# Kernel optimization log

Hardware: AMD Instinct MI355X
Metric: run time of the kernel (lower is better)

The kernel has to match this reference:

```python
import jax, jax.numpy as jnp
import numpy as np

B, S, d, D = 128, 1024, 64, 64  # batch, seq_len, physical dim, bond dim


def setup_inputs() -> dict:
    key = jax.random.key(0)
    k1, k2, k3, k4 = jax.random.split(key, 4)
    k_core = (d * D * D) ** (-0.5)
    k_vec = d ** (-0.5)
    core = k_core * jax.random.normal(k1, (d, D, D), dtype=jnp.float32)
    left_boundary = k_vec * jax.random.normal(k2, (D,), dtype=jnp.float32)
    right_boundary = k_vec * jax.random.normal(k3, (D,), dtype=jnp.float32)
    X = jax.random.randint(k4, (B, S), 0, d, dtype=jnp.int32)
    return {"X": X, "core": core, "left_boundary": left_boundary,
            "right_boundary": right_boundary}


def reference(X, core, left_boundary, right_boundary):
    """Faithful JAX version of TTrain._log_contract_at_batch (homogeneous).

    X: [B, S] int category indices; core: [d, D, D]; boundaries: [D].
    Returns logprobs: [B].
    The per-step normalization (infinity-norm) + accumulated log-norm trick of
    the original is preserved exactly; the final
    log((exp(lognorm) * out)**2) is computed in the mathematically identical
    stable form 2*(lognorm + log|out|).
    """
    batch = X.shape[0]
    lb = jnp.broadcast_to(left_boundary, (batch, left_boundary.shape[0]))  # [B, D]
    Z0 = jnp.max(jnp.abs(lb), axis=1)                                      # [B]
    c0 = lb / Z0[:, None]
    logn0 = jnp.log(Z0)

    def step(carry, x_t):
        c, logn = carry                       # c: [B, D]
        w_t = core[x_t]                       # gather selected cores: [B, D, D]
        ct = jnp.einsum('bi,bij->bj', c, w_t)  # [B, D]
        Zt = jnp.max(jnp.abs(ct), axis=1)      # [B] infinity norm
        return (ct / Zt[:, None], logn + jnp.log(Zt)), None

    (c, logn), _ = jax.lax.scan(step, (c0, logn0), X.T)  # scan over seq axis
    out = jnp.einsum('bi,i->b', c, right_boundary)        # [B]
    logprobs = 2.0 * (logn + jnp.log(jnp.abs(out)))
    return logprobs
```

## Files before the change

kernel.cpp:

```cpp
#include <hip/hip_runtime.h>
#include <math.h>


#define TT_S 1024
#define TT_D 64

typedef __attribute__((ext_vector_type(8))) short short8;
typedef __attribute__((ext_vector_type(4))) float float4v;
typedef __attribute__((ext_vector_type(4))) unsigned uint4v;

static __device__ __forceinline__ short8 as_short8(uint4v u) {
    union { uint4v u; short8 s; } x; x.u = u; return x.s;
}

__global__ __launch_bounds__(64) void tt_prep(
    const float* __restrict__ core, short* __restrict__ tblA,
    short* __restrict__ tblBt)
{
    const int x = blockIdx.x, l = threadIdx.x;
    const int n = l & 15, q = l >> 4;
    const float* W = core + x * 4096;

    #pragma unroll
    for (int I = 0; I < 4; ++I)
        #pragma unroll
        for (int Kp = 0; Kp < 2; ++Kp) {
            short8 v;
            const int row = 16 * I + n;
            const int c0 = 32 * Kp + 4 * q;
            #pragma unroll
            for (int j = 0; j < 8; ++j) {
                const int col = c0 + 16 * (j >> 2) + (j & 3);
                v[j] = (short)(__float_as_uint(W[row * 64 + col]) >> 16);
            }
            *(short8*)(tblA + ((size_t)(x * 8 + I * 2 + Kp) * 64 + l) * 8) = v;
        }
    #pragma unroll
    for (int Kp = 0; Kp < 2; ++Kp)
        #pragma unroll
        for (int J = 0; J < 4; ++J) {
            short8 v;
            const int col = 16 * J + n;
            const int r0 = 32 * Kp + 4 * q;
            #pragma unroll
            for (int j = 0; j < 8; ++j) {
                const int row = r0 + 16 * (j >> 2) + (j & 3);
                v[j] = (short)(__float_as_uint(W[row * 64 + col]) >> 16);
            }
            *(short8*)(tblBt + ((size_t)(x * 8 + Kp * 4 + J) * 64 + l) * 8) = v;
        }
}

__global__ __launch_bounds__(64, 2) void tt_stage1(
    const int* __restrict__ X, const short* __restrict__ tblA,
    const short* __restrict__ tblBt, float* __restrict__ PT,
    float* __restrict__ ln1)
{
    const int w = blockIdx.x;
    const int b = w >> 4, chunk = w & 15;
    const int l = threadIdx.x, n = l & 15, q = l >> 4;
    const int* Xc = X + b * TT_S + chunk * 64;

    const float4v zero = {0.f, 0.f, 0.f, 0.f};
    float4v acc[4][4];
    short8 Bf[8], A0[8], A1[8];
    float logn = 0.f;

    #define LOAD_FRAGS(DST, TBL, XIDX)                                        \
    {   const short8* p_ = (const short8*)((TBL) + (size_t)(XIDX) * 4096) + l; \
        _Pragma("unroll")                                                     \
        for (int f_ = 0; f_ < 8; ++f_) (DST)[f_] = p_[f_ * 64]; }

    #define MFMA_ALL(ABUF)                                                    \
        _Pragma("unroll")                                                     \
        for (int I_ = 0; I_ < 4; ++I_)                                        \
            _Pragma("unroll")                                                 \
            for (int J_ = 0; J_ < 4; ++J_) {                                  \
                float4v c0_ = __builtin_amdgcn_mfma_f32_16x16x32_bf16(        \
                    (ABUF)[2 * I_ + 0], Bf[J_], zero, 0, 0, 0);               \
                acc[I_][J_] = __builtin_amdgcn_mfma_f32_16x16x32_bf16(        \
                    (ABUF)[2 * I_ + 1], Bf[4 + J_], c0_, 0, 0, 0);            \
            }

    #define PACK_BF()                                                         \
        _Pragma("unroll")                                                     \
        for (int Kp_ = 0; Kp_ < 2; ++Kp_)                                     \
            _Pragma("unroll")                                                 \
            for (int J_ = 0; J_ < 4; ++J_) {                                  \
                uint4v u_;                                                    \
                u_[0] = __builtin_amdgcn_perm(                                \
                    __float_as_uint(acc[2 * Kp_][J_][1]),                     \
                    __float_as_uint(acc[2 * Kp_][J_][0]), 0x07060302u);       \
                u_[1] = __builtin_amdgcn_perm(                                \
                    __float_as_uint(acc[2 * Kp_][J_][3]),                     \
                    __float_as_uint(acc[2 * Kp_][J_][2]), 0x07060302u);       \
                u_[2] = __builtin_amdgcn_perm(                                \
                    __float_as_uint(acc[2 * Kp_ + 1][J_][1]),                 \
                    __float_as_uint(acc[2 * Kp_ + 1][J_][0]), 0x07060302u);   \
                u_[3] = __builtin_amdgcn_perm(                                \
                    __float_as_uint(acc[2 * Kp_ + 1][J_][3]),                 \
                    __float_as_uint(acc[2 * Kp_ + 1][J_][2]), 0x07060302u);   \
                Bf[Kp_ * 4 + J_] = as_short8(u_);                             \
            }

    #define RENORM()                                                          \
    {   float Z_ = 0.f;                                                       \
        _Pragma("unroll")                                                     \
        for (int I_ = 0; I_ < 4; ++I_)                                        \
            _Pragma("unroll")                                                 \
            for (int J_ = 0; J_ < 4; ++J_)                                    \
                _Pragma("unroll")                                             \
                for (int r_ = 0; r_ < 4; ++r_)                                \
                    Z_ = fmaxf(Z_, fabsf(acc[I_][J_][r_]));                   \
        _Pragma("unroll")                                                     \
        for (int m_ = 32; m_; m_ >>= 1) Z_ = fmaxf(Z_, __shfl_xor(Z_, m_));   \
        logn += logf(Z_);                                                     \
        const float rZ_ = 1.0f / Z_;                                          \
        _Pragma("unroll")                                                     \
        for (int I_ = 0; I_ < 4; ++I_)                                        \
            _Pragma("unroll")                                                 \
            for (int J_ = 0; J_ < 4; ++J_)                                    \
                _Pragma("unroll")                                             \
                for (int r_ = 0; r_ < 4; ++r_) acc[I_][J_][r_] *= rZ_; }

    LOAD_FRAGS(Bf, tblBt, Xc[63])
    LOAD_FRAGS(A0, tblA, Xc[62])
    LOAD_FRAGS(A1, tblA, Xc[61])

    MFMA_ALL(A0)
    LOAD_FRAGS(A0, tblA, Xc[60])

    #pragma unroll 1
    for (int it = 0; it < 31; ++it) {
        PACK_BF()
        MFMA_ALL(A1)
        {
            const int tn = 59 - 2 * it;
            LOAD_FRAGS(A1, tblA, Xc[tn < 0 ? 0 : tn])
        }
        if (((2 * it + 2) & 7) == 0) RENORM()
        PACK_BF()
        MFMA_ALL(A0)
        {
            const int tn = 58 - 2 * it;
            LOAD_FRAGS(A0, tblA, Xc[tn < 0 ? 0 : tn])
        }
    }

    {
        float Z = 0.f;
        #pragma unroll
        for (int I = 0; I < 4; ++I)
            #pragma unroll
            for (int J = 0; J < 4; ++J)
                #pragma unroll
                for (int r = 0; r < 4; ++r) Z = fmaxf(Z, fabsf(acc[I][J][r]));
        #pragma unroll
        for (int m = 32; m; m >>= 1) Z = fmaxf(Z, __shfl_xor(Z, m));
        logn += logf(Z);
        const float rZ = 1.0f / Z;
        float* base = PT + (size_t)w * 4096;
        #pragma unroll
        for (int I = 0; I < 4; ++I)
            #pragma unroll
            for (int J = 0; J < 4; ++J) {
                float4v v = acc[I][J];
                #pragma unroll
                for (int r = 0; r < 4; ++r) v[r] *= rZ;
                *(float4v*)(base + (16 * J + n) * 64 + 16 * I + 4 * q) = v;
            }
        if (l == 0) ln1[w] = logn;
    }
    #undef LOAD_FRAGS
    #undef MFMA_ALL
    #undef PACK_BF
    #undef RENORM
}

__global__ __launch_bounds__(64) void tt_stage2(
    const float* __restrict__ PT, const float* __restrict__ ln1,
    const float* __restrict__ lb, const float* __restrict__ rb,
    float* __restrict__ out)
{
    __shared__ float cb[64];
    const int b = blockIdx.x, j = threadIdx.x;

    float c = lb[j];
    float Z = fabsf(c);
    #pragma unroll
    for (int m = 32; m; m >>= 1) Z = fmaxf(Z, __shfl_xor(Z, m));
    float logn = logf(Z);
    c *= (1.0f / Z);

    float ln = (j < 16) ? ln1[b * 16 + j] : 0.f;
    #pragma unroll
    for (int m = 32; m; m >>= 1) ln += __shfl_xor(ln, m);
    logn += ln;

    const float* base = PT + (size_t)b * 16 * 4096 + j * 64;
    float4v wb[16];
    #pragma unroll
    for (int f = 0; f < 16; ++f) wb[f] = ((const float4v*)base)[f];

    #pragma unroll 1
    for (int k = 0; k < 16; ++k) {
        float4v wn[16];
        const float4v* nb = (const float4v*)(base + (size_t)((k + 1) & 15) * 4096);
        #pragma unroll
        for (int f = 0; f < 16; ++f) wn[f] = nb[f];

        cb[j] = c;
        asm volatile("s_waitcnt lgkmcnt(0)" ::: "memory");
        float a0 = 0.f, a1 = 0.f, a2 = 0.f, a3 = 0.f;
        #pragma unroll
        for (int f = 0; f < 16; ++f) {
            const float4v cv = *(const float4v*)(cb + 4 * f);
            a0 = fmaf(cv[0], wb[f][0], a0);
            a1 = fmaf(cv[1], wb[f][1], a1);
            a2 = fmaf(cv[2], wb[f][2], a2);
            a3 = fmaf(cv[3], wb[f][3], a3);
        }
        float cn = (a0 + a1) + (a2 + a3);
        float Zl = fabsf(cn);
        #pragma unroll
        for (int m = 32; m; m >>= 1) Zl = fmaxf(Zl, __shfl_xor(Zl, m));
        logn += logf(Zl);
        c = cn * (1.0f / Zl);
        #pragma unroll
        for (int f = 0; f < 16; ++f) wb[f] = wn[f];
    }

    float dot = c * rb[j];
    #pragma unroll
    for (int m = 32; m; m >>= 1) dot += __shfl_xor(dot, m);
    if (j == 0) out[b] = 2.0f * (logn + logf(fabsf(dot)));
}

__global__ __launch_bounds__(256) void tt_transpose(
    const float* __restrict__ core, float* __restrict__ coreT)
{
    __shared__ float tile[64][65];
    const int x = blockIdx.x;
    const float* src = core + x * 4096;
    float* dst = coreT + x * 4096;
    const int r0 = threadIdx.x >> 6, cc = threadIdx.x & 63;
    #pragma unroll
    for (int k = 0; k < 16; ++k) tile[r0 + 4 * k][cc] = src[(r0 + 4 * k) * 64 + cc];
    __syncthreads();
    #pragma unroll
    for (int k = 0; k < 16; ++k) dst[(r0 + 4 * k) * 64 + cc] = tile[cc][r0 + 4 * k];
}

__global__ __launch_bounds__(64, 1) void ttrain_chain2(
    const int* __restrict__ X, const float* __restrict__ coreT,
    const float* __restrict__ lb, const float* __restrict__ rb,
    float* __restrict__ out)
{
    __shared__ float cbuf[2][64];
    const int b = blockIdx.x, j = threadIdx.x;
    const int* Xrow = X + b * TT_S;
    float c = lb[j];
    float Z = fabsf(c);
    #pragma unroll
    for (int m = 32; m; m >>= 1) Z = fmaxf(Z, __shfl_xor(Z, m));
    float logn = logf(Z);
    c *= (1.0f / Z);
    const float* colbase = coreT + j * 64;
    int xs_cur = Xrow[j];
    int xs_nxt = Xrow[64 + j];
    float4 wA[16], wB[16];
    {
        const int x0 = Xrow[0];
        const float4* p = (const float4*)(colbase + x0 * 4096);
        #pragma unroll
        for (int k = 0; k < 16; ++k) wA[k] = p[k];
    }
    #define TT_STEP(WCUR, WNXT, SLOT, XNEXT, T)                              \
    {                                                                        \
        cbuf[SLOT][j] = c;                                                   \
        {                                                                    \
            const float4* pre = (const float4*)(colbase + (XNEXT) * 4096);   \
            _Pragma("unroll")                                                \
            for (int k = 0; k < 16; ++k) WNXT[k] = pre[k];                   \
        }                                                                    \
        asm volatile("s_waitcnt lgkmcnt(0)" ::: "memory");                   \
        float a0 = 0.f, a1 = 0.f, a2 = 0.f, a3 = 0.f;                        \
        const float4* cb2 = (const float4*)cbuf[SLOT];                       \
        _Pragma("unroll")                                                    \
        for (int k = 0; k < 16; ++k) {                                       \
            float4 cv = cb2[k];                                              \
            a0 = fmaf(cv.x, WCUR[k].x, a0);                                  \
            a1 = fmaf(cv.y, WCUR[k].y, a1);                                  \
            a2 = fmaf(cv.z, WCUR[k].z, a2);                                  \
            a3 = fmaf(cv.w, WCUR[k].w, a3);                                  \
        }                                                                    \
        float cn = (a0 + a1) + (a2 + a3);                                    \
        if (((T) & 7) == 7) {                                                \
            float Zl = fabsf(cn);                                            \
            _Pragma("unroll")                                                \
            for (int m = 32; m; m >>= 1) Zl = fmaxf(Zl, __shfl_xor(Zl, m));  \
            logn += logf(Zl);                                                \
            cn *= (1.0f / Zl);                                               \
        }                                                                    \
        c = cn;                                                              \
    }
    for (int tc = 0; tc < TT_S; tc += 64) {
        #pragma unroll 1
        for (int u = 0; u < 64; u += 2) {
            const int x1 = __builtin_amdgcn_readlane(xs_cur, u + 1);
            TT_STEP(wA, wB, 0, x1, tc + u)
            const int src2 = (u + 2 < 64) ? xs_cur : xs_nxt;
            const int x2 = __builtin_amdgcn_readlane(src2, (u + 2) & 63);
            TT_STEP(wB, wA, 1, x2, tc + u + 1)
        }
        xs_cur = xs_nxt;
        const int nc = tc + 128;
        xs_nxt = Xrow[((nc < TT_S) ? nc : 0) + j];
    }
    #undef TT_STEP
    float dot = c * rb[j];
    #pragma unroll
    for (int m = 32; m; m >>= 1) dot += __shfl_xor(dot, m);
    if (j == 0) out[b] = 2.0f * (logn + logf(fabsf(dot)));
}

extern "C" void kernel_launch(void* const* d_in, const int* in_sizes, int n_in,
                              void* d_out, int out_size, void* d_ws, size_t ws_size,
                              hipStream_t stream) {
    const int*   X    = (const int*)d_in[0];
    const float* core = (const float*)d_in[1];
    const float* lb   = (const float*)d_in[2];
    const float* rb   = (const float*)d_in[3];
    float* out = (float*)d_out;

    const int B = in_sizes[0] / TT_S;
    const size_t tblBytes = (size_t)64 * 8 * 64 * 8 * sizeof(short);
    const size_t ptBytes  = (size_t)B * 16 * 4096 * sizeof(float);
    const size_t lnBytes  = (size_t)B * 16 * sizeof(float);
    const size_t need = 2 * tblBytes + ptBytes + lnBytes;

    if (ws_size >= need) {
        char* w = (char*)d_ws;
        short* tblA  = (short*)w;
        short* tblBt = (short*)(w + tblBytes);
        float* PT    = (float*)(w + 2 * tblBytes);
        float* ln1   = (float*)(w + 2 * tblBytes + ptBytes);
        tt_prep<<<64, 64, 0, stream>>>(core, tblA, tblBt);
        tt_stage1<<<B * 16, 64, 0, stream>>>(X, tblA, tblBt, PT, ln1);
        tt_stage2<<<B, 64, 0, stream>>>(PT, ln1, lb, rb, out);
    } else if (ws_size >= (size_t)64 * 4096 * sizeof(float)) {
        float* coreT = (float*)d_ws;
        tt_transpose<<<64, 256, 0, stream>>>(core, coreT);
        ttrain_chain2<<<B, TT_D, 0, stream>>>(X, coreT, lb, rb, out);
    }
}
```

Baseline: 143.8 us.

## Split sequence into 32 chunks, store partial products in bf16, double-buffer stage2

```diff
diff --git a/kernel.cpp b/kernel.cpp
--- a/kernel.cpp
+++ b/kernel.cpp
@@ -4,10 +4,13 @@
 
 #define TT_S 1024
 #define TT_D 64
+#define NCHUNK 32
+#define CLEN 32
 
 typedef __attribute__((ext_vector_type(8))) short short8;
 typedef __attribute__((ext_vector_type(4))) float float4v;
 typedef __attribute__((ext_vector_type(4))) unsigned uint4v;
+typedef __attribute__((ext_vector_type(2))) unsigned uint2v;
 
 static __device__ __forceinline__ short8 as_short8(uint4v u) {
     union { uint4v u; short8 s; } x; x.u = u; return x.s;
@@ -51,19 +54,19 @@
         }
 }
 
-__global__ __launch_bounds__(64, 2) void tt_stage1(
+__global__ __launch_bounds__(64, 4) void tt_stage1(
     const int* __restrict__ X, const short* __restrict__ tblA,
-    const short* __restrict__ tblBt, float* __restrict__ PT,
+    const short* __restrict__ tblBt, short* __restrict__ PT,
     float* __restrict__ ln1)
 {
     const int w = blockIdx.x;
-    const int b = w >> 4, chunk = w & 15;
+    const int b = w / NCHUNK, chunk = w % NCHUNK;
     const int l = threadIdx.x, n = l & 15, q = l >> 4;
-    const int* Xc = X + b * TT_S + chunk * 64;
+    const int* Xc = X + b * TT_S + chunk * CLEN;
 
     const float4v zero = {0.f, 0.f, 0.f, 0.f};
     float4v acc[4][4];
-    short8 Bf[8], A0[8], A1[8];
+    short8 Bf[8], Af[8];
     float logn = 0.f;
 
     #define LOAD_FRAGS(DST, TBL, XIDX)                                        \
@@ -123,28 +126,17 @@
                 _Pragma("unroll")                                             \
                 for (int r_ = 0; r_ < 4; ++r_) acc[I_][J_][r_] *= rZ_; }
 
-    LOAD_FRAGS(Bf, tblBt, Xc[63])
-    LOAD_FRAGS(A0, tblA, Xc[62])
-    LOAD_FRAGS(A1, tblA, Xc[61])
-
-    MFMA_ALL(A0)
-    LOAD_FRAGS(A0, tblA, Xc[60])
+    LOAD_FRAGS(Bf, tblBt, Xc[CLEN - 1])
+    LOAD_FRAGS(Af, tblA, Xc[CLEN - 2])
+    MFMA_ALL(Af)
 
     #pragma unroll 1
-    for (int it = 0; it < 31; ++it) {
+    for (int s = 1; s < CLEN - 1; ++s) {
+        LOAD_FRAGS(Af, tblA, Xc[CLEN - 2 - s])
+        asm volatile("" ::: "memory");
+        if ((s & 7) == 0) RENORM()
         PACK_BF()
-        MFMA_ALL(A1)
-        {
-            const int tn = 59 - 2 * it;
-            LOAD_FRAGS(A1, tblA, Xc[tn < 0 ? 0 : tn])
-        }
-        if (((2 * it + 2) & 7) == 0) RENORM()
-        PACK_BF()
-        MFMA_ALL(A0)
-        {
-            const int tn = 58 - 2 * it;
-            LOAD_FRAGS(A0, tblA, Xc[tn < 0 ? 0 : tn])
-        }
+        MFMA_ALL(Af)
     }
 
     {
@@ -159,7 +151,7 @@
         for (int m = 32; m; m >>= 1) Z = fmaxf(Z, __shfl_xor(Z, m));
         logn += logf(Z);
         const float rZ = 1.0f / Z;
-        float* base = PT + (size_t)w * 4096;
+        short* base = PT + (size_t)w * 4096;
         #pragma unroll
         for (int I = 0; I < 4; ++I)
             #pragma unroll
@@ -167,7 +159,12 @@
                 float4v v = acc[I][J];
                 #pragma unroll
                 for (int r = 0; r < 4; ++r) v[r] *= rZ;
-                *(float4v*)(base + (16 * J + n) * 64 + 16 * I + 4 * q) = v;
+                uint2v dd;
+                dd[0] = __builtin_amdgcn_perm(__float_as_uint(v[1]),
+                                              __float_as_uint(v[0]), 0x07060302u);
+                dd[1] = __builtin_amdgcn_perm(__float_as_uint(v[3]),
+                                              __float_as_uint(v[2]), 0x07060302u);
+                *(uint2v*)(base + (16 * J + n) * 64 + 16 * I + 4 * q) = dd;
             }
         if (l == 0) ln1[w] = logn;
     }
@@ -177,8 +174,8 @@
     #undef RENORM
 }
 
-__global__ __launch_bounds__(64) void tt_stage2(
-    const float* __restrict__ PT, const float* __restrict__ ln1,
+__global__ __launch_bounds__(64, 1) void tt_stage2(
+    const short* __restrict__ PT, const float* __restrict__ ln1,
     const float* __restrict__ lb, const float* __restrict__ rb,
     float* __restrict__ out)
 {
@@ -192,43 +189,61 @@
     float logn = logf(Z);
     c *= (1.0f / Z);
 
-    float ln = (j < 16) ? ln1[b * 16 + j] : 0.f;
+    float ln = (j < NCHUNK) ? ln1[b * NCHUNK + j] : 0.f;
     #pragma unroll
     for (int m = 32; m; m >>= 1) ln += __shfl_xor(ln, m);
     logn += ln;
 
-    const float* base = PT + (size_t)b * 16 * 4096 + j * 64;
-    float4v wb[16];
-    #pragma unroll
-    for (int f = 0; f < 16; ++f) wb[f] = ((const float4v*)base)[f];
+    const short* base = PT + (size_t)b * NCHUNK * 4096 + j * 64;
+
+    short8 bufA[8], bufB[8];
+    #pragma unroll
+    for (int f = 0; f < 8; ++f) bufA[f] = ((const short8*)base)[f];
+
+    #define S2_STEP(BUF)                                                      \
+    {                                                                         \
+        cb[j] = c;                                                            \
+        asm volatile("s_waitcnt lgkmcnt(0)" ::: "memory");                    \
+        float a0 = 0.f, a1 = 0.f, a2 = 0.f, a3 = 0.f;                         \
+        _Pragma("unroll")                                                     \
+        for (int f = 0; f < 8; ++f) {                                         \
+            union { short8 s; uint4v u; } uu; uu.s = (BUF)[f];                \
+            const float4v cv0 = *(const float4v*)(cb + 8 * f);                \
+            const float4v cv1 = *(const float4v*)(cb + 8 * f + 4);            \
+            a0 = fmaf(cv0[0], __uint_as_float(uu.u[0] << 16), a0);            \
+            a1 = fmaf(cv0[1], __uint_as_float(uu.u[0] & 0xffff0000u), a1);    \
+            a2 = fmaf(cv0[2], __uint_as_float(uu.u[1] << 16), a2);            \
+            a3 = fmaf(cv0[3], __uint_as_float(uu.u[1] & 0xffff0000u), a3);    \
+            a0 = fmaf(cv1[0], __uint_as_float(uu.u[2] << 16), a0);            \
+            a1 = fmaf(cv1[1], __uint_as_float(uu.u[2] & 0xffff0000u), a1);    \
+            a2 = fmaf(cv1[2], __uint_as_float(uu.u[3] << 16), a2);            \
+            a3 = fmaf(cv1[3], __uint_as_float(uu.u[3] & 0xffff0000u), a3);    \
+        }                                                                     \
+        float cn = (a0 + a1) + (a2 + a3);                                     \
+        float Zl = fabsf(cn);                                                 \
+        _Pragma("unroll")                                                     \
+        for (int m = 32; m; m >>= 1) Zl = fmaxf(Zl, __shfl_xor(Zl, m));       \
+        logn += logf(Zl);                                                     \
+        c = cn * (1.0f / Zl);                                                 \
+    }
 
     #pragma unroll 1
-    for (int k = 0; k < 16; ++k) {
-        float4v wn[16];
-        const float4v* nb = (const float4v*)(base + (size_t)((k + 1) & 15) * 4096);
-        #pragma unroll
-        for (int f = 0; f < 16; ++f) wn[f] = nb[f];
-
-        cb[j] = c;
-        asm volatile("s_waitcnt lgkmcnt(0)" ::: "memory");
-        float a0 = 0.f, a1 = 0.f, a2 = 0.f, a3 = 0.f;
-        #pragma unroll
-        for (int f = 0; f < 16; ++f) {
-            const float4v cv = *(const float4v*)(cb + 4 * f);
-            a0 = fmaf(cv[0], wb[f][0], a0);
-            a1 = fmaf(cv[1], wb[f][1], a1);
-            a2 = fmaf(cv[2], wb[f][2], a2);
-            a3 = fmaf(cv[3], wb[f][3], a3);
-        }
-        float cn = (a0 + a1) + (a2 + a3);
-        float Zl = fabsf(cn);
-        #pragma unroll
-        for (int m = 32; m; m >>= 1) Zl = fmaxf(Zl, __shfl_xor(Zl, m));
-        logn += logf(Zl);
-        c = cn * (1.0f / Zl);
-        #pragma unroll
-        for (int f = 0; f < 16; ++f) wb[f] = wn[f];
-    }
+    for (int k = 0; k < NCHUNK; k += 2) {
+        {   const short8* p = (const short8*)(base + (size_t)(k + 1) * 4096);
+            #pragma unroll
+            for (int f = 0; f < 8; ++f) bufB[f] = p[f];
+        }
+        asm volatile("" ::: "memory");
+        S2_STEP(bufA)
+        {   const int kn = (k + 2 < NCHUNK) ? (k + 2) : (NCHUNK - 1);
+            const short8* p = (const short8*)(base + (size_t)kn * 4096);
+            #pragma unroll
+            for (int f = 0; f < 8; ++f) bufA[f] = p[f];
+        }
+        asm volatile("" ::: "memory");
+        S2_STEP(bufB)
+    }
+    #undef S2_STEP
 
     float dot = c * rb[j];
     #pragma unroll
@@ -335,18 +350,18 @@
 
     const int B = in_sizes[0] / TT_S;
     const size_t tblBytes = (size_t)64 * 8 * 64 * 8 * sizeof(short);
-    const size_t ptBytes  = (size_t)B * 16 * 4096 * sizeof(float);
-    const size_t lnBytes  = (size_t)B * 16 * sizeof(float);
+    const size_t ptBytes  = (size_t)B * NCHUNK * 4096 * sizeof(short);
+    const size_t lnBytes  = (size_t)B * NCHUNK * sizeof(float);
     const size_t need = 2 * tblBytes + ptBytes + lnBytes;
 
     if (ws_size >= need) {
         char* w = (char*)d_ws;
         short* tblA  = (short*)w;
         short* tblBt = (short*)(w + tblBytes);
-        float* PT    = (float*)(w + 2 * tblBytes);
+        short* PT    = (short*)(w + 2 * tblBytes);
         float* ln1   = (float*)(w + 2 * tblBytes + ptBytes);
         tt_prep<<<64, 64, 0, stream>>>(core, tblA, tblBt);
-        tt_stage1<<<B * 16, 64, 0, stream>>>(X, tblA, tblBt, PT, ln1);
+        tt_stage1<<<B * NCHUNK, 64, 0, stream>>>(X, tblA, tblBt, PT, ln1);
         tt_stage2<<<B, 64, 0, stream>>>(PT, ln1, lb, rb, out);
     } else if (ws_size >= (size_t)64 * 4096 * sizeof(float)) {
         float* coreT = (float*)d_ws;
```

After: 154.0 us. +7.1%, slower.
